# Optimization experiments

Measured on AMD Instinct MI355X. Metric: run time of the kernel, lower is better.

## Reference

```python
import jax, jax.numpy as jnp
import numpy as np

EPS = 1e-5

def _layernorm(x, g, b):
    mu = jnp.mean(x, axis=-1, keepdims=True)
    var = jnp.mean(jnp.square(x - mu), axis=-1, keepdims=True)
    return (x - mu) * jax.lax.rsqrt(var + EPS) * g + b

def _time_shift(x):
    # xx[:, t] = x[:, t-1], xx[:, 0] = 0  (ZeroPad2d((0,0,1,-1)))
    return jnp.pad(x, ((0, 0), (1, 0), (0, 0)))[:, :-1, :]

def _wkv(time_decay, time_first, k, v):
    # Numerically-stable RWKV v4 recurrence (matches wkv_cuda forward).
    # k, v: [B, T, C]; time_decay, time_first: [C]
    w = -jnp.exp(time_decay)  # negative decay
    u = time_first
    B, T, C = k.shape
    aa0 = jnp.zeros((B, C), k.dtype)
    bb0 = jnp.zeros((B, C), k.dtype)
    pp0 = jnp.full((B, C), -1e38, k.dtype)

    def step(carry, kv_t):
        aa, bb, pp = carry
        kt, vt = kv_t
        ww = u + kt
        p = jnp.maximum(pp, ww)
        e1 = jnp.exp(pp - p)
        e2 = jnp.exp(ww - p)
        yt = (e1 * aa + e2 * vt) / (e1 * bb + e2)
        ww2 = pp + w
        p2 = jnp.maximum(ww2, kt)
        e1b = jnp.exp(ww2 - p2)
        e2b = jnp.exp(kt - p2)
        return (e1b * aa + e2b * vt, e1b * bb + e2b, p2), yt

    kT = jnp.swapaxes(k, 0, 1)  # [T, B, C]
    vT = jnp.swapaxes(v, 0, 1)
    _, y = jax.lax.scan(step, (aa0, bb0, pp0), (kT, vT))
    return jnp.swapaxes(y, 0, 1)  # [B, T, C]


def setup_inputs() -> dict:
    num_layers, layer_id, C = 8, 1, 512
    B, T = 512, 50
    H = 4 * C
    key = jax.random.key(0)
    ks = jax.random.split(key, 12)

    # parameter init mirroring the torch module's structured init
    ratio_0_to_1 = layer_id / (num_layers - 1)
    ratio_1_to_almost0 = 1.0 - layer_id / num_layers
    h = np.arange(C, dtype=np.float32)
    time_decay = (-5 + 8 * (h / (C - 1)) ** (0.7 + 1.3 * ratio_0_to_1)).astype(np.float32)
    zigzag = (np.array([(i + 1) % 3 - 1 for i in range(C)], dtype=np.float32)) * 0.5
    time_first = (np.ones(C, dtype=np.float32) * np.log(0.3) + zigzag).astype(np.float32)
    xr = (h / C).astype(np.float32)
    att_mix_k = (xr ** ratio_1_to_almost0)[None, None, :].astype(np.float32)
    att_mix_v = (xr ** ratio_1_to_almost0 + 0.3 * ratio_0_to_1)[None, None, :].astype(np.float32)
    att_mix_r = (xr ** (0.5 * ratio_1_to_almost0))[None, None, :].astype(np.float32)
    ffn_mix_k = att_mix_k.copy()
    ffn_mix_r = att_mix_k.copy()

    s = 0.02
    return {
        "x": jax.random.normal(ks[0], (B, T, C), jnp.float32),
        "ln1_g": jnp.ones((C,), jnp.float32), "ln1_b": jnp.zeros((C,), jnp.float32),
        "ln2_g": jnp.ones((C,), jnp.float32), "ln2_b": jnp.zeros((C,), jnp.float32),
        "att_mix_k": jnp.asarray(att_mix_k), "att_mix_v": jnp.asarray(att_mix_v),
        "att_mix_r": jnp.asarray(att_mix_r),
        "time_decay": jnp.asarray(time_decay), "time_first": jnp.asarray(time_first),
        "Wk": jax.random.normal(ks[1], (C, C), jnp.float32) * s,
        "Wv": jax.random.normal(ks[2], (C, C), jnp.float32) * s,
        "Wr": jax.random.normal(ks[3], (C, C), jnp.float32) * s,
        "Wo": jax.random.normal(ks[4], (C, C), jnp.float32) * s,
        "ffn_mix_k": jnp.asarray(ffn_mix_k), "ffn_mix_r": jnp.asarray(ffn_mix_r),
        "Fk": jax.random.normal(ks[5], (H, C), jnp.float32) * s,
        "Fv": jax.random.normal(ks[6], (C, H), jnp.float32) * s,
        "Fr": jax.random.normal(ks[7], (C, C), jnp.float32) * s,
    }


def reference(x, ln1_g, ln1_b, ln2_g, ln2_b,
              att_mix_k, att_mix_v, att_mix_r, time_decay, time_first,
              Wk, Wv, Wr, Wo, ffn_mix_k, ffn_mix_r, Fk, Fv, Fr):
    # --- time-mix (attention) branch ---
    h = _layernorm(x, ln1_g, ln1_b)
    hh = _time_shift(h)
    xk = h * att_mix_k + hh * (1 - att_mix_k)
    xv = h * att_mix_v + hh * (1 - att_mix_v)
    xr = h * att_mix_r + hh * (1 - att_mix_r)
    k = jnp.einsum('btc,dc->btd', xk, Wk)
    v = jnp.einsum('btc,dc->btd', xv, Wv)
    sr = jax.nn.sigmoid(jnp.einsum('btc,dc->btd', xr, Wr))
    rwkv = sr * _wkv(time_decay, time_first, k, v)
    x = x + jnp.einsum('btc,dc->btd', rwkv, Wo)

    # --- channel-mix (FFN) branch ---
    h = _layernorm(x, ln2_g, ln2_b)
    hh = _time_shift(h)
    fk = h * ffn_mix_k + hh * (1 - ffn_mix_k)
    fr = h * ffn_mix_r + hh * (1 - ffn_mix_r)
    kk = jnp.einsum('btc,hc->bth', fk, Fk)
    kk = jnp.square(jax.nn.relu(kk))
    kv = jnp.einsum('bth,ch->btc', kk, Fv)
    rkv = jax.nn.sigmoid(jnp.einsum('btc,dc->btd', fr, Fr)) * kv
    return x + rkv
```

## Files before the change

### kernel.cpp

```cpp
#include <hip/hip_runtime.h>
#include <stdint.h>

typedef unsigned short u16;
typedef __bf16 bf16x8 __attribute__((ext_vector_type(8)));
typedef float f32x4 __attribute__((ext_vector_type(4)));

#define DEV static __device__ __forceinline__

DEV u16 f2b(float f) {
    unsigned u = __float_as_uint(f);
    u += 0x7FFF + ((u >> 16) & 1);
    return (u16)(u >> 16);
}
DEV float b2f(u16 h) { return __uint_as_float((unsigned)h << 16); }

DEV void load16(const void* g, void* l) {
    __builtin_amdgcn_global_load_lds((const __attribute__((address_space(1))) void*)g,
                                     (__attribute__((address_space(3))) void*)l, 16, 0, 0);
}

__global__ __launch_bounds__(256) void cvt_bf16(const float* __restrict__ src,
                                                u16* __restrict__ dst, int n) {
    int i = (blockIdx.x * 256 + threadIdx.x) * 4;
    if (i < n) {
        float4 f = *(const float4*)(src + i);
        ushort4 o;
        o.x = f2b(f.x); o.y = f2b(f.y); o.z = f2b(f.z); o.w = f2b(f.w);
        *(ushort4*)(dst + i) = o;
    }
}

template <int NOUT>
__global__ __launch_bounds__(256) void ln_mix(
    const float* __restrict__ x, const float* __restrict__ g, const float* __restrict__ be,
    const float* __restrict__ mk, const float* __restrict__ mv, const float* __restrict__ mr,
    u16* __restrict__ ok, u16* __restrict__ ov, u16* __restrict__ orr, int T) {
    const int C = 512;
    int row = blockIdx.x;
    int t = row % T;
    int tid = threadIdx.x;
    int c = tid * 2;
    const float* xt = x + (size_t)row * C;
    float2 vt = *(const float2*)(xt + c);
    float2 vp = make_float2(0.f, 0.f);
    if (t > 0) vp = *(const float2*)(xt - C + c);

    float s0 = vt.x + vt.y, s1 = vt.x * vt.x + vt.y * vt.y;
    float s2 = vp.x + vp.y, s3 = vp.x * vp.x + vp.y * vp.y;
#pragma unroll
    for (int off = 32; off; off >>= 1) {
        s0 += __shfl_down(s0, off); s1 += __shfl_down(s1, off);
        s2 += __shfl_down(s2, off); s3 += __shfl_down(s3, off);
    }
    __shared__ float sm[16];
    int w = tid >> 6;
    if ((tid & 63) == 0) { sm[w*4+0] = s0; sm[w*4+1] = s1; sm[w*4+2] = s2; sm[w*4+3] = s3; }
    __syncthreads();
    s0 = sm[0] + sm[4] + sm[8]  + sm[12];
    s1 = sm[1] + sm[5] + sm[9]  + sm[13];
    s2 = sm[2] + sm[6] + sm[10] + sm[14];
    s3 = sm[3] + sm[7] + sm[11] + sm[15];

    const float rC = 1.f / 512.f;
    float mu_t = s0 * rC, var_t = s1 * rC - mu_t * mu_t;
    float mu_p = s2 * rC, var_p = s3 * rC - mu_p * mu_p;
    float rs_t = rsqrtf(var_t + 1e-5f);
    float rs_p = rsqrtf(var_p + 1e-5f);

    float xk0[2], xv0[2], xr0[2];
#pragma unroll
    for (int j = 0; j < 2; ++j) {
        int cc = c + j;
        float gg = g[cc], bb = be[cc];
        float xv_ = (j ? vt.y : vt.x);
        float xp_ = (j ? vp.y : vp.x);
        float h  = (xv_ - mu_t) * rs_t * gg + bb;
        float hh = (t > 0) ? ((xp_ - mu_p) * rs_p * gg + bb) : 0.f;
        float a = mk[cc];
        xk0[j] = h * a + hh * (1.f - a);
        if (NOUT == 3) { float av = mv[cc]; xv0[j] = h * av + hh * (1.f - av); }
        float ar = mr[cc];
        xr0[j] = h * ar + hh * (1.f - ar);
    }
    size_t idx = (size_t)row * C + c;
    *(ushort2*)&ok[idx] = make_ushort2(f2b(xk0[0]), f2b(xk0[1]));
    if (NOUT == 3) *(ushort2*)&ov[idx] = make_ushort2(f2b(xv0[0]), f2b(xv0[1]));
    *(ushort2*)&orr[idx] = make_ushort2(f2b(xr0[0]), f2b(xr0[1]));
}

template <int EPI>
__global__ __launch_bounds__(256) void gemm_nt(
    const u16* __restrict__ A, const u16* __restrict__ B, void* __restrict__ Out,
    const float* __restrict__ Add, const u16* __restrict__ Mul, int K, int D) {
    const int BM = 128, BN = 128, BK = 32;
    __shared__ __align__(16) u16 As[BM * BK];
    __shared__ __align__(16) u16 Bs[BN * BK];
    int tid = threadIdx.x;
    int lane = tid & 63;
    int w = tid >> 6;
    int wm = w >> 1, wn = w & 1;
    int rowBase = blockIdx.y * BM;
    int colBase = blockIdx.x * BN;
    int lrow = lane >> 2;
    int lk = (lane & 3) * 8;

    f32x4 acc[4][4] = {};

    const int nk = K / BK;
    for (int kt = 0; kt < nk; ++kt) {
        int kBase = kt * BK;
#pragma unroll
        for (int i = 0; i < 2; ++i) {
            int r0 = w * 32 + i * 16;
            const u16* gA = A + (size_t)(rowBase + r0 + lrow) * K + kBase + lk;
            load16(gA, &As[r0 * BK]);
            const u16* gB = B + (size_t)(colBase + r0 + lrow) * K + kBase + lk;
            load16(gB, &Bs[r0 * BK]);
        }
        __syncthreads();
        bf16x8 af[4], bfr[4];
#pragma unroll
        for (int m = 0; m < 4; ++m)
            af[m] = *(const bf16x8*)&As[(wm * 64 + m * 16 + (lane & 15)) * BK + (lane >> 4) * 8];
#pragma unroll
        for (int n = 0; n < 4; ++n)
            bfr[n] = *(const bf16x8*)&Bs[(wn * 64 + n * 16 + (lane & 15)) * BK + (lane >> 4) * 8];
#pragma unroll
        for (int m = 0; m < 4; ++m)
#pragma unroll
            for (int n = 0; n < 4; ++n)
                acc[m][n] = __builtin_amdgcn_mfma_f32_16x16x32_bf16(af[m], bfr[n], acc[m][n], 0, 0, 0);
        __syncthreads();
    }

    int r0 = (lane >> 4) * 4;
    int cc = lane & 15;
#pragma unroll
    for (int m = 0; m < 4; ++m) {
#pragma unroll
        for (int n = 0; n < 4; ++n) {
            int row = rowBase + wm * 64 + m * 16 + r0;
            int col = colBase + wn * 64 + n * 16 + cc;
#pragma unroll
            for (int r = 0; r < 4; ++r) {
                size_t idx = (size_t)(row + r) * D + col;
                float v = acc[m][n][r];
                if (EPI == 0) {
                    ((u16*)Out)[idx] = f2b(v);
                } else if (EPI == 1) {
                    ((u16*)Out)[idx] = f2b(1.f / (1.f + __expf(-v)));
                } else if (EPI == 2) {
                    ((float*)Out)[idx] = v + Add[idx];
                } else if (EPI == 3) {
                    float rr = fmaxf(v, 0.f);
                    ((u16*)Out)[idx] = f2b(rr * rr);
                } else {
                    float s = 1.f / (1.f + __expf(-v));
                    ((float*)Out)[idx] = Add[idx] + s * b2f(Mul[idx]);
                }
            }
        }
    }
}

__global__ __launch_bounds__(256) void wkv_kernel(
    const u16* __restrict__ k, const u16* __restrict__ v, const u16* __restrict__ sr,
    const float* __restrict__ td, const float* __restrict__ tf,
    u16* __restrict__ rwkv, int T) {
    const int C = 512;
    int gid = blockIdx.x * 256 + threadIdx.x;
    int c = gid & (C - 1);
    int b = gid >> 9;
    float w = -__expf(td[c]);
    float u = tf[c];
    float aa = 0.f, bb = 0.f, pp = -1e38f;
    size_t idx = (size_t)b * T * C + c;
    for (int t = 0; t < T; ++t, idx += C) {
        float kt = b2f(k[idx]), vt = b2f(v[idx]);
        float ww = u + kt;
        float p = fmaxf(pp, ww);
        float e1 = __expf(pp - p), e2 = __expf(ww - p);
        float y = (e1 * aa + e2 * vt) / (e1 * bb + e2);
        float ww2 = pp + w;
        float p2 = fmaxf(ww2, kt);
        float e1b = __expf(ww2 - p2), e2b = __expf(kt - p2);
        aa = e1b * aa + e2b * vt;
        bb = e1b * bb + e2b;
        pp = p2;
        rwkv[idx] = f2b(b2f(sr[idx]) * y);
    }
}

extern "C" void kernel_launch(void* const* d_in, const int* in_sizes, int n_in,
                              void* d_out, int out_size, void* d_ws, size_t ws_size,
                              hipStream_t stream) {
    const int B = 512, T = 50, C = 512, H = 2048;
    const int NT = B * T;

    const float* x     = (const float*)d_in[0];
    const float* ln1_g = (const float*)d_in[1];
    const float* ln1_b = (const float*)d_in[2];
    const float* ln2_g = (const float*)d_in[3];
    const float* ln2_b = (const float*)d_in[4];
    const float* amk   = (const float*)d_in[5];
    const float* amv   = (const float*)d_in[6];
    const float* amr   = (const float*)d_in[7];
    const float* td    = (const float*)d_in[8];
    const float* tf    = (const float*)d_in[9];
    const float* Wk    = (const float*)d_in[10];
    const float* Wv    = (const float*)d_in[11];
    const float* Wr    = (const float*)d_in[12];
    const float* Wo    = (const float*)d_in[13];
    const float* fmk   = (const float*)d_in[14];
    const float* fmr   = (const float*)d_in[15];
    const float* Fk    = (const float*)d_in[16];
    const float* Fv    = (const float*)d_in[17];
    const float* Fr    = (const float*)d_in[18];
    float* out = (float*)d_out;

    const size_t WBYTES = ((size_t)C*C*2)*5 + ((size_t)H*C*2)*2 + 4096;
    int R = 6400;
    if (ws_size >= (size_t)25600 * 1024 * 7 + WBYTES)      R = 25600;
    else if (ws_size >= (size_t)12800 * 1024 * 7 + WBYTES) R = 12800;
    const int NCH = NT / R;

    char* ws = (char*)d_ws;
    size_t off = 0;
    auto alloc = [&](size_t bytes) {
        char* p = ws + off;
        off += (bytes + 255) & ~(size_t)255;
        return p;
    };
    const size_t uc = (size_t)R * C * 2;
    u16*   U0 = (u16*)alloc(uc);
    u16*   U1 = (u16*)alloc(uc);
    u16*   U2 = (u16*)alloc(uc);
    u16*   U3 = (u16*)alloc(uc);
    u16*   U4 = (u16*)alloc(uc);
    float* X2 = (float*)alloc((size_t)R * C * 4);
    u16* bWk = (u16*)alloc((size_t)C * C * 2);
    u16* bWv = (u16*)alloc((size_t)C * C * 2);
    u16* bWr = (u16*)alloc((size_t)C * C * 2);
    u16* bWo = (u16*)alloc((size_t)C * C * 2);
    u16* bFk = (u16*)alloc((size_t)H * C * 2);
    u16* bFv = (u16*)alloc((size_t)C * H * 2);
    u16* bFr = (u16*)alloc((size_t)C * C * 2);
    u16* kk = U0;

    cvt_bf16<<<C * C / 1024, 256, 0, stream>>>(Wk, bWk, C * C);
    cvt_bf16<<<C * C / 1024, 256, 0, stream>>>(Wv, bWv, C * C);
    cvt_bf16<<<C * C / 1024, 256, 0, stream>>>(Wr, bWr, C * C);
    cvt_bf16<<<C * C / 1024, 256, 0, stream>>>(Wo, bWo, C * C);
    cvt_bf16<<<H * C / 1024, 256, 0, stream>>>(Fk, bFk, H * C);
    cvt_bf16<<<C * H / 1024, 256, 0, stream>>>(Fv, bFv, C * H);
    cvt_bf16<<<C * C / 1024, 256, 0, stream>>>(Fr, bFr, C * C);

    for (int ch = 0; ch < NCH; ++ch) {
        const float* xc  = x   + (size_t)ch * R * C;
        float*       oc  = out + (size_t)ch * R * C;
        dim3 g512(C / 128, R / 128);
        dim3 gH (H / 128, R / 256);
        dim3 gKV(C / 128, R / 256);

        ln_mix<3><<<R, 256, 0, stream>>>(xc, ln1_g, ln1_b, amk, amv, amr, U0, U1, U2, T);
        gemm_nt<0><<<g512, 256, 0, stream>>>(U0, bWk, U3, nullptr, nullptr, C, C);
        gemm_nt<0><<<g512, 256, 0, stream>>>(U1, bWv, U4, nullptr, nullptr, C, C);
        gemm_nt<1><<<g512, 256, 0, stream>>>(U2, bWr, U1, nullptr, nullptr, C, C);
        wkv_kernel<<<(R / T) * C / 256, 256, 0, stream>>>(U3, U4, U1, td, tf, U0, T);
        gemm_nt<2><<<g512, 256, 0, stream>>>(U0, bWo, X2, xc, nullptr, C, C);

        ln_mix<2><<<R, 256, 0, stream>>>(X2, ln2_g, ln2_b, fmk, nullptr, fmr, U3, nullptr, U4, T);
        for (int hhalf = 0; hhalf < 2; ++hhalf) {
            size_t ro = (size_t)hhalf * (R / 2);
            gemm_nt<3><<<gH,  256, 0, stream>>>(U3 + ro * C, bFk, kk, nullptr, nullptr, C, H);
            gemm_nt<0><<<gKV, 256, 0, stream>>>(kk, bFv, U2 + ro * C, nullptr, nullptr, H, C);
        }
        gemm_nt<4><<<g512, 256, 0, stream>>>(U4, bFr, oc, X2, U2, C, C);
    }
}
```

Measured before the change: 624.7 us.

## Rework GEMM tiling with swizzled LDS, block remap, and batched k/v/r projection

Replaces the 128x128x32 GEMM with a templated 64xBN kernel using BK=64. It adds an XOR-swizzled LDS layout meant to avoid bank conflicts on fragment reads, and remaps block IDs in interleaved groups of 8 to improve cache locality across dies. The three time-mix projections (k, v, sigmoid r) become one launch over grid.z, using concatenated bf16 weights and contiguous input buffers. The sr output is stored in the X2 buffer, which is free at that point. Smaller output tiles give more blocks and better occupancy, but each block reuses its loaded tiles less.

```diff
diff --git a/kernel.cpp b/kernel.cpp
--- a/kernel.cpp
+++ b/kernel.cpp
@@ -88,75 +88,110 @@
     *(ushort2*)&orr[idx] = make_ushort2(f2b(xr0[0]), f2b(xr0[1]));
 }
 
-template <int EPI>
-__global__ __launch_bounds__(256) void gemm_nt(
-    const u16* __restrict__ A, const u16* __restrict__ B, void* __restrict__ Out,
-    const float* __restrict__ Add, const u16* __restrict__ Mul, int K, int D) {
-    const int BM = 128, BN = 128, BK = 32;
+template <int BN, int EPI>
+__global__ __launch_bounds__(256) void gemm64(
+    const u16* __restrict__ A0, int strideAz,
+    const u16* __restrict__ B0, int strideBz,
+    void* O0, void* O1, void* O2,
+    const float* __restrict__ Add, const u16* __restrict__ Mul,
+    int K, int D) {
+    const int BM = 64, BK = 64;
+    const int NT_ = BN / 32;
     __shared__ __align__(16) u16 As[BM * BK];
     __shared__ __align__(16) u16 Bs[BN * BK];
+
+    int gx = gridDim.x, gy = gridDim.y;
+    int fid = blockIdx.x + gx * (blockIdx.y + gy * blockIdx.z);
+    int nwg = gx * gy * gridDim.z;
+    int swz = (fid & 7) * (nwg >> 3) + (fid >> 3);
+    int bx = swz % gx;
+    int tmp = swz / gx;
+    int by = tmp % gy;
+    int bz = tmp / gy;
+
+    const u16* A = A0 + (size_t)bz * strideAz;
+    const u16* B = B0 + (size_t)bz * strideBz;
+    void* Out = (bz == 0) ? O0 : (bz == 1) ? O1 : O2;
+
     int tid = threadIdx.x;
     int lane = tid & 63;
     int w = tid >> 6;
     int wm = w >> 1, wn = w & 1;
-    int rowBase = blockIdx.y * BM;
-    int colBase = blockIdx.x * BN;
-    int lrow = lane >> 2;
-    int lk = (lane & 3) * 8;
-
-    f32x4 acc[4][4] = {};
-
-    const int nk = K / BK;
-    for (int kt = 0; kt < nk; ++kt) {
-        int kBase = kt * BK;
+    int rowBase = by * BM;
+    int colBase = bx * BN;
+    int l8 = lane >> 3;
+    int gsrc = ((lane & 7) ^ l8) * 8;
+
+    f32x4 acc[2][NT_] = {};
+
+    for (int kt = 0; kt < K; kt += BK) {
 #pragma unroll
         for (int i = 0; i < 2; ++i) {
-            int r0 = w * 32 + i * 16;
-            const u16* gA = A + (size_t)(rowBase + r0 + lrow) * K + kBase + lk;
-            load16(gA, &As[r0 * BK]);
-            const u16* gB = B + (size_t)(colBase + r0 + lrow) * K + kBase + lk;
-            load16(gB, &Bs[r0 * BK]);
+            int r0 = w * 16 + i * 8;
+            load16(A + (size_t)(rowBase + r0 + l8) * K + kt + gsrc, &As[r0 * BK]);
+        }
+#pragma unroll
+        for (int i = 0; i < BN / 32; ++i) {
+            int r0 = w * (BN / 4) + i * 8;
+            load16(B + (size_t)(colBase + r0 + l8) * K + kt + gsrc, &Bs[r0 * BK]);
         }
         __syncthreads();
-        bf16x8 af[4], bfr[4];
-#pragma unroll
-        for (int m = 0; m < 4; ++m)
-            af[m] = *(const bf16x8*)&As[(wm * 64 + m * 16 + (lane & 15)) * BK + (lane >> 4) * 8];
-#pragma unroll
-        for (int n = 0; n < 4; ++n)
-            bfr[n] = *(const bf16x8*)&Bs[(wn * 64 + n * 16 + (lane & 15)) * BK + (lane >> 4) * 8];
-#pragma unroll
-        for (int m = 0; m < 4; ++m)
-#pragma unroll
-            for (int n = 0; n < 4; ++n)
-                acc[m][n] = __builtin_amdgcn_mfma_f32_16x16x32_bf16(af[m], bfr[n], acc[m][n], 0, 0, 0);
+
+        bf16x8 af[2][2], bfr[NT_][2];
+#pragma unroll
+        for (int m = 0; m < 2; ++m) {
+            int row = wm * 32 + m * 16 + (lane & 15);
+            int rx = row & 7;
+#pragma unroll
+            for (int s = 0; s < 2; ++s) {
+                int gsw = (s * 4 + (lane >> 4)) ^ rx;
+                af[m][s] = *(const bf16x8*)&As[row * BK + gsw * 8];
+            }
+        }
+#pragma unroll
+        for (int n = 0; n < NT_; ++n) {
+            int col = wn * (BN / 2) + n * 16 + (lane & 15);
+            int rx = col & 7;
+#pragma unroll
+            for (int s = 0; s < 2; ++s) {
+                int gsw = (s * 4 + (lane >> 4)) ^ rx;
+                bfr[n][s] = *(const bf16x8*)&Bs[col * BK + gsw * 8];
+            }
+        }
+#pragma unroll
+        for (int s = 0; s < 2; ++s)
+#pragma unroll
+            for (int m = 0; m < 2; ++m)
+#pragma unroll
+                for (int n = 0; n < NT_; ++n)
+                    acc[m][n] = __builtin_amdgcn_mfma_f32_16x16x32_bf16(af[m][s], bfr[n][s], acc[m][n], 0, 0, 0);
         __syncthreads();
     }
 
-    int r0 = (lane >> 4) * 4;
-    int cc = lane & 15;
-#pragma unroll
-    for (int m = 0; m < 4; ++m) {
-#pragma unroll
-        for (int n = 0; n < 4; ++n) {
-            int row = rowBase + wm * 64 + m * 16 + r0;
-            int col = colBase + wn * 64 + n * 16 + cc;
+    int r0e = (lane >> 4) * 4;
+    int ce = lane & 15;
+#pragma unroll
+    for (int m = 0; m < 2; ++m) {
+#pragma unroll
+        for (int n = 0; n < NT_; ++n) {
+            int row = rowBase + wm * 32 + m * 16 + r0e;
+            int col = colBase + wn * (BN / 2) + n * 16 + ce;
 #pragma unroll
             for (int r = 0; r < 4; ++r) {
                 size_t idx = (size_t)(row + r) * D + col;
                 float v = acc[m][n][r];
                 if (EPI == 0) {
                     ((u16*)Out)[idx] = f2b(v);
-                } else if (EPI == 1) {
-                    ((u16*)Out)[idx] = f2b(1.f / (1.f + __expf(-v)));
                 } else if (EPI == 2) {
                     ((float*)Out)[idx] = v + Add[idx];
                 } else if (EPI == 3) {
                     float rr = fmaxf(v, 0.f);
                     ((u16*)Out)[idx] = f2b(rr * rr);
-                } else {
+                } else if (EPI == 4) {
                     float s = 1.f / (1.f + __expf(-v));
                     ((float*)Out)[idx] = Add[idx] + s * b2f(Mul[idx]);
+                } else {
+                    ((u16*)Out)[idx] = (bz == 2) ? f2b(1.f / (1.f + __expf(-v))) : f2b(v);
                 }
             }
         }
@@ -218,7 +253,7 @@
     const float* Fr    = (const float*)d_in[18];
     float* out = (float*)d_out;
 
-    const size_t WBYTES = ((size_t)C*C*2)*5 + ((size_t)H*C*2)*2 + 4096;
+    const size_t WBYTES = ((size_t)C*C*2)*6 + ((size_t)H*C*2)*2 + 4096;
     int R = 6400;
     if (ws_size >= (size_t)25600 * 1024 * 7 + WBYTES)      R = 25600;
     else if (ws_size >= (size_t)12800 * 1024 * 7 + WBYTES) R = 12800;
@@ -238,18 +273,17 @@
     u16*   U3 = (u16*)alloc(uc);
     u16*   U4 = (u16*)alloc(uc);
     float* X2 = (float*)alloc((size_t)R * C * 4);
-    u16* bWk = (u16*)alloc((size_t)C * C * 2);
-    u16* bWv = (u16*)alloc((size_t)C * C * 2);
-    u16* bWr = (u16*)alloc((size_t)C * C * 2);
-    u16* bWo = (u16*)alloc((size_t)C * C * 2);
-    u16* bFk = (u16*)alloc((size_t)H * C * 2);
-    u16* bFv = (u16*)alloc((size_t)C * H * 2);
-    u16* bFr = (u16*)alloc((size_t)C * C * 2);
+    u16*   U5 = (u16*)X2;
+    u16* bWkvr = (u16*)alloc((size_t)3 * C * C * 2);
+    u16* bWo   = (u16*)alloc((size_t)C * C * 2);
+    u16* bFk   = (u16*)alloc((size_t)H * C * 2);
+    u16* bFv   = (u16*)alloc((size_t)C * H * 2);
+    u16* bFr   = (u16*)alloc((size_t)C * C * 2);
     u16* kk = U0;
 
-    cvt_bf16<<<C * C / 1024, 256, 0, stream>>>(Wk, bWk, C * C);
-    cvt_bf16<<<C * C / 1024, 256, 0, stream>>>(Wv, bWv, C * C);
-    cvt_bf16<<<C * C / 1024, 256, 0, stream>>>(Wr, bWr, C * C);
+    cvt_bf16<<<C * C / 1024, 256, 0, stream>>>(Wk, bWkvr,             C * C);
+    cvt_bf16<<<C * C / 1024, 256, 0, stream>>>(Wv, bWkvr + C * C,     C * C);
+    cvt_bf16<<<C * C / 1024, 256, 0, stream>>>(Wr, bWkvr + 2 * C * C, C * C);
     cvt_bf16<<<C * C / 1024, 256, 0, stream>>>(Wo, bWo, C * C);
     cvt_bf16<<<H * C / 1024, 256, 0, stream>>>(Fk, bFk, H * C);
     cvt_bf16<<<C * H / 1024, 256, 0, stream>>>(Fv, bFv, C * H);
@@ -258,23 +292,23 @@
     for (int ch = 0; ch < NCH; ++ch) {
         const float* xc  = x   + (size_t)ch * R * C;
         float*       oc  = out + (size_t)ch * R * C;
-        dim3 g512(C / 128, R / 128);
-        dim3 gH (H / 128, R / 256);
-        dim3 gKV(C / 128, R / 256);
 
         ln_mix<3><<<R, 256, 0, stream>>>(xc, ln1_g, ln1_b, amk, amv, amr, U0, U1, U2, T);
-        gemm_nt<0><<<g512, 256, 0, stream>>>(U0, bWk, U3, nullptr, nullptr, C, C);
-        gemm_nt<0><<<g512, 256, 0, stream>>>(U1, bWv, U4, nullptr, nullptr, C, C);
-        gemm_nt<1><<<g512, 256, 0, stream>>>(U2, bWr, U1, nullptr, nullptr, C, C);
-        wkv_kernel<<<(R / T) * C / 256, 256, 0, stream>>>(U3, U4, U1, td, tf, U0, T);
-        gemm_nt<2><<<g512, 256, 0, stream>>>(U0, bWo, X2, xc, nullptr, C, C);
+        gemm64<128, 5><<<dim3(C / 128, R / 64, 3), 256, 0, stream>>>(
+            U0, R * C, bWkvr, C * C, U3, U4, U5, nullptr, nullptr, C, C);
+        wkv_kernel<<<(R / T) * C / 256, 256, 0, stream>>>(U3, U4, U5, td, tf, U0, T);
+        gemm64<128, 2><<<dim3(C / 128, R / 64, 1), 256, 0, stream>>>(
+            U0, 0, bWo, 0, X2, nullptr, nullptr, xc, nullptr, C, C);
 
         ln_mix<2><<<R, 256, 0, stream>>>(X2, ln2_g, ln2_b, fmk, nullptr, fmr, U3, nullptr, U4, T);
-        for (int hhalf = 0; hhalf < 2; ++hhalf) {
-            size_t ro = (size_t)hhalf * (R / 2);
-            gemm_nt<3><<<gH,  256, 0, stream>>>(U3 + ro * C, bFk, kk, nullptr, nullptr, C, H);
-            gemm_nt<0><<<gKV, 256, 0, stream>>>(kk, bFv, U2 + ro * C, nullptr, nullptr, H, C);
-        }
-        gemm_nt<4><<<g512, 256, 0, stream>>>(U4, bFr, oc, X2, U2, C, C);
-    }
-}
+        for (int hh = 0; hh < 2; ++hh) {
+            size_t ro = (size_t)hh * (R / 2);
+            gemm64<128, 3><<<dim3(H / 128, R / 128, 1), 256, 0, stream>>>(
+                U3 + ro * C, 0, bFk, 0, kk, nullptr, nullptr, nullptr, nullptr, C, H);
+            gemm64<64, 0><<<dim3(C / 64, R / 128, 1), 256, 0, stream>>>(
+                kk, 0, bFv, 0, U2 + ro * C, nullptr, nullptr, nullptr, nullptr, H, C);
+        }
+        gemm64<128, 4><<<dim3(C / 128, R / 64, 1), 256, 0, stream>>>(
+            U4, 0, bFr, 0, oc, nullptr, nullptr, X2, U2, C, C);
+    }
+}
```

Measured after the change: 540.9 us. 1.15x faster.
